# Kernel optimization log

Measured on AMD Instinct MI355X. Metric: run time of the kernel, lower is better.

The kernel has to match this reference:

```python
import jax, jax.numpy as jnp
import numpy as np

N_ITEMS = 30000
N_USERS = 20000
N_NODES = N_ITEMS + N_USERS  # 50000
N_EDGES = 512000
D0, D1, D2 = 768, 128, 64
EPS = 1e-12  # torch F.normalize eps


def _xavier(key, shape):
    fan_in, fan_out = shape
    bound = np.sqrt(6.0 / (fan_in + fan_out)).astype(np.float32)
    return jax.random.uniform(key, shape, jnp.float32, -bound, bound)


def setup_inputs() -> dict:
    key = jax.random.key(0)
    ks = jax.random.split(key, 12)
    return {
        "item_embed": jax.random.normal(ks[0], (N_ITEMS, D0), jnp.float32) * 0.05,
        "user_embed": jax.random.normal(ks[1], (N_USERS, D0), jnp.float32) * 0.05,
        "W1_0": _xavier(ks[2], (D0, D1)),
        "b1_0": jnp.zeros((D1,), jnp.float32),
        "W2_0": _xavier(ks[3], (D0, D1)),
        "b2_0": jnp.zeros((D1,), jnp.float32),
        "W1_1": _xavier(ks[4], (D1, D2)),
        "b1_1": jnp.zeros((D2,), jnp.float32),
        "W2_1": _xavier(ks[5], (D1, D2)),
        "b2_1": jnp.zeros((D2,), jnp.float32),
        # normalized-Laplacian-like positive edge weights
        "edge_vals": jax.random.uniform(ks[6], (N_EDGES,), jnp.float32) * 0.1,
        "edge_rows": jax.random.randint(ks[7], (N_EDGES,), 0, N_NODES, jnp.int32),
        "edge_cols": jax.random.randint(ks[8], (N_EDGES,), 0, N_NODES, jnp.int32),
    }


def _ngcf_layer(ego, edge_vals, edge_rows, edge_cols, W1, b1, W2, b2):
    # side = A_in @ ego : gather source features, scale, segment-sum into rows
    msg = edge_vals[:, None] * ego[edge_cols]            # (E, d) gather
    side = jax.ops.segment_sum(msg, edge_rows, num_segments=N_NODES)
    side_plus_I = side + ego                             # (A + I) @ ego
    simple = side_plus_I @ W1 + b1                       # linear1
    interaction = (side * ego) @ W2 + b2                 # linear2 on Hadamard
    return jax.nn.leaky_relu(simple + interaction)       # dropout = eval/no-op


def reference(item_embed, user_embed, W1_0, b1_0, W2_0, b2_0,
              W1_1, b1_1, W2_1, b2_1, edge_vals, edge_rows, edge_cols):
    ego = jnp.concatenate([item_embed, user_embed], axis=0)  # (N, 768)
    all_embed = [ego]
    for (W1, b1, W2, b2) in ((W1_0, b1_0, W2_0, b2_0), (W1_1, b1_1, W2_1, b2_1)):
        ego = _ngcf_layer(ego, edge_vals, edge_rows, edge_cols, W1, b1, W2, b2)
        norm = jnp.maximum(jnp.linalg.norm(ego, axis=1, keepdims=True), EPS)
        all_embed.append(ego / norm)
    return jnp.concatenate(all_embed, axis=1)  # (N, 768+128+64)
```

## Files before the change

kernel.cpp:

```cpp
#include <hip/hip_runtime.h>
#include <stdint.h>

#define N_ITEMS 30000
#define N_USERS 20000
#define N_NODES 50000
#define N_EDGES 512000
#define D0 768
#define D1 128
#define D2 64
#define OSTRIDE 960

typedef short bf16x8 __attribute__((ext_vector_type(8)));
typedef float f32x4  __attribute__((ext_vector_type(4)));
typedef unsigned short u16x4 __attribute__((ext_vector_type(4)));
typedef unsigned short u16x2 __attribute__((ext_vector_type(2)));

__device__ __forceinline__ unsigned short f2bf(float x) {
    union { float f; uint32_t u; } v; v.f = x;
    uint32_t u = v.u;
    return (unsigned short)((u + 0x7FFF + ((u >> 16) & 1)) >> 16);
}
__device__ __forceinline__ float bf2f(unsigned short s) {
    union { uint32_t u; float f; } v; v.u = ((uint32_t)s) << 16; return v.f;
}

__global__ __launch_bounds__(256) void copy_ego0(const float* __restrict__ item,
                                                 const float* __restrict__ user,
                                                 float* __restrict__ out,
                                                 unsigned short* __restrict__ outb) {
    int idx = blockIdx.x * 256 + threadIdx.x;
    if (idx >= N_NODES * (D0 / 4)) return;
    int row = idx / (D0 / 4);
    int c4  = idx % (D0 / 4);
    const float4* src = (row < N_ITEMS)
        ? (const float4*)(item + (size_t)row * D0)
        : (const float4*)(user + (size_t)(row - N_ITEMS) * D0);
    float4 v = src[c4];
    *(float4*)(out + (size_t)row * OSTRIDE + c4 * 4) = v;
    if (outb) {
        u16x4 b;
        b[0] = f2bf(v.x); b[1] = f2bf(v.y); b[2] = f2bf(v.z); b[3] = f2bf(v.w);
        *(u16x4*)(outb + (size_t)row * D0 + c4 * 4) = b;
    }
}

__global__ __launch_bounds__(256) void histogram_kernel(const int* __restrict__ rows,
                                                        int* __restrict__ counts) {
    int e = blockIdx.x * 256 + threadIdx.x;
    if (e < N_EDGES) atomicAdd(&counts[rows[e]], 1);
}

#define SCAN_THREADS 1024
__global__ __launch_bounds__(1024) void scan_kernel(const int* __restrict__ counts,
                                                    int* __restrict__ offsets,
                                                    int* __restrict__ cursors) {
    __shared__ int partials[SCAN_THREADS];
    const int CH = (N_NODES + SCAN_THREADS - 1) / SCAN_THREADS;
    int t = threadIdx.x;
    int base = t * CH;
    int sum = 0;
    for (int i = 0; i < CH; i++) {
        int idx = base + i;
        if (idx < N_NODES) sum += counts[idx];
    }
    partials[t] = sum;
    __syncthreads();
    for (int off = 1; off < SCAN_THREADS; off <<= 1) {
        int add = (t >= off) ? partials[t - off] : 0;
        __syncthreads();
        partials[t] += add;
        __syncthreads();
    }
    int run = (t == 0) ? 0 : partials[t - 1];
    for (int i = 0; i < CH; i++) {
        int idx = base + i;
        if (idx < N_NODES) {
            offsets[idx] = run;
            cursors[idx] = run;
            run += counts[idx];
        }
    }
    if (t == SCAN_THREADS - 1) offsets[N_NODES] = N_EDGES;
}

__global__ __launch_bounds__(256) void fill_kernel(const float* __restrict__ vals,
                                                   const int* __restrict__ rows,
                                                   const int* __restrict__ cols,
                                                   int* __restrict__ cursors,
                                                   float* __restrict__ svals,
                                                   int* __restrict__ scols) {
    int e = blockIdx.x * 256 + threadIdx.x;
    if (e >= N_EDGES) return;
    int pos = atomicAdd(&cursors[rows[e]], 1);
    svals[pos] = vals[e];
    scols[pos] = cols[e];
}

template <int K, int N>
__global__ __launch_bounds__(256) void prep_wb(const float* __restrict__ W,
                                               unsigned short* __restrict__ Wb) {
    constexpr int FR = (K / 32) * (N / 16);
    int tid = blockIdx.x * 256 + threadIdx.x;
    if (tid >= FR * 64) return;
    int frag = tid >> 6, lane = tid & 63;
    int kk = frag / (N / 16), nt = frag % (N / 16);
    int quad = lane >> 4, n = lane & 15;
    unsigned short tmp[8];
#pragma unroll
    for (int jj = 0; jj < 8; jj++) {
        int k = kk * 32 + quad * 8 + jj;
        tmp[jj] = f2bf(W[(size_t)k * N + nt * 16 + n]);
    }
#pragma unroll
    for (int jj = 0; jj < 8; jj++) Wb[(size_t)tid * 8 + jj] = tmp[jj];
}

template <int DIN, int DOUT, int THREADS, bool BSRC>
__global__ __launch_bounds__(THREADS) void fused_layer_mfma(
    const int*   __restrict__ offsets,
    const float* __restrict__ svals,
    const int*   __restrict__ scols,
    const float* __restrict__ ego, int ego_stride,
    const unsigned short* __restrict__ egob,
    const unsigned short* __restrict__ Wb1,
    const unsigned short* __restrict__ Wb2,
    const float* __restrict__ b1, const float* __restrict__ b2,
    float* __restrict__ out, int out_stride,
    unsigned short* __restrict__ outb)
{
    constexpr int NPB   = 16;
    constexpr int WAVES = THREADS / 64;
    constexpr int NPW   = NPB / WAVES;
    constexpr int KK    = DIN / 32;
    constexpr int NT    = DOUT / 16;
    constexpr int NTW   = NT / WAVES;
    constexpr int PAD   = 8;
    constexpr int CW    = (DIN >= 256) ? 4 : 2;
    constexpr int NC    = DIN / (64 * CW);

    __shared__ unsigned short s_sum [NPB][DIN + PAD];
    __shared__ unsigned short s_prod[NPB][DIN + PAD];

    const int t = threadIdx.x;
    const int w = t >> 6, l = t & 63;
    const int node_base = blockIdx.x * NPB;

    for (int nn = 0; nn < NPW; nn++) {
        int n   = w * NPW + nn;
        int row = node_base + n;
        int beg = offsets[row], end = offsets[row + 1];
        float acc[NC * CW];
#pragma unroll
        for (int c = 0; c < NC * CW; c++) acc[c] = 0.f;

        auto gather_one = [&](int gc, float v) {
            if constexpr (BSRC) {
                const unsigned short* sp = egob + (size_t)gc * DIN;
#pragma unroll
                for (int c = 0; c < NC; c++) {
                    if constexpr (CW == 4) {
                        u16x4 q = *(const u16x4*)(sp + c * 256 + l * 4);
#pragma unroll
                        for (int j = 0; j < 4; j++)
                            acc[c * 4 + j] = fmaf(v, bf2f(q[j]), acc[c * 4 + j]);
                    } else {
                        u16x2 q = *(const u16x2*)(sp + l * 2);
                        acc[0] = fmaf(v, bf2f(q[0]), acc[0]);
                        acc[1] = fmaf(v, bf2f(q[1]), acc[1]);
                    }
                }
            } else {
                const float* sp = ego + (size_t)gc * ego_stride;
#pragma unroll
                for (int c = 0; c < NC; c++) {
                    if constexpr (CW == 4) {
                        float4 q = *(const float4*)(sp + c * 256 + l * 4);
                        acc[c * 4 + 0] = fmaf(v, q.x, acc[c * 4 + 0]);
                        acc[c * 4 + 1] = fmaf(v, q.y, acc[c * 4 + 1]);
                        acc[c * 4 + 2] = fmaf(v, q.z, acc[c * 4 + 2]);
                        acc[c * 4 + 3] = fmaf(v, q.w, acc[c * 4 + 3]);
                    } else {
                        float2 q = *(const float2*)(sp + l * 2);
                        acc[0] = fmaf(v, q.x, acc[0]);
                        acc[1] = fmaf(v, q.y, acc[1]);
                    }
                }
            }
        };

        for (int base = beg; base < end; base += 64) {
            int cnt = min(64, end - base);
            int   cl = 0;
            float vl = 0.f;
            if (l < cnt) { cl = scols[base + l]; vl = svals[base + l]; }
            int u = 0;
            for (; u + 1 < cnt; u += 2) {
                int   g0 = __shfl(cl, u),     g1 = __shfl(cl, u + 1);
                float v0 = __shfl(vl, u),     v1 = __shfl(vl, u + 1);
                gather_one(g0, v0);
                gather_one(g1, v1);
            }
            if (u < cnt) gather_one(__shfl(cl, u), __shfl(vl, u));
        }

#pragma unroll
        for (int c = 0; c < NC; c++) {
            if constexpr (CW == 4) {
                float4 e4 = *(const float4*)(ego + (size_t)row * ego_stride + c * 256 + l * 4);
                float eg[4] = {e4.x, e4.y, e4.z, e4.w};
                u16x4 s, p;
#pragma unroll
                for (int j = 0; j < 4; j++) {
                    float a = acc[c * 4 + j];
                    s[j] = f2bf(a + eg[j]);
                    p[j] = f2bf(a * eg[j]);
                }
                *(u16x4*)&s_sum [n][c * 256 + l * 4] = s;
                *(u16x4*)&s_prod[n][c * 256 + l * 4] = p;
            } else {
                float2 e2 = *(const float2*)(ego + (size_t)row * ego_stride + l * 2);
                u16x2 s, p;
                s[0] = f2bf(acc[0] + e2.x); p[0] = f2bf(acc[0] * e2.x);
                s[1] = f2bf(acc[1] + e2.y); p[1] = f2bf(acc[1] * e2.y);
                *(u16x2*)&s_sum [n][l * 2] = s;
                *(u16x2*)&s_prod[n][l * 2] = p;
            }
        }
    }
    __syncthreads();

    const int m = l & 15, quad = l >> 4;
    f32x4 accc[NTW] = {};
    for (int kk = 0; kk < KK; kk++) {
        bf16x8 a_s = *(const bf16x8*)&s_sum [m][kk * 32 + quad * 8];
        bf16x8 a_p = *(const bf16x8*)&s_prod[m][kk * 32 + quad * 8];
#pragma unroll
        for (int i = 0; i < NTW; i++) {
            int nt = w * NTW + i;
            bf16x8 bf1 = *(const bf16x8*)(Wb1 + ((size_t)(kk * NT + nt) * 64 + l) * 8);
            bf16x8 bf2 = *(const bf16x8*)(Wb2 + ((size_t)(kk * NT + nt) * 64 + l) * 8);
            accc[i] = __builtin_amdgcn_mfma_f32_16x16x32_bf16(a_s, bf1, accc[i], 0, 0, 0);
            accc[i] = __builtin_amdgcn_mfma_f32_16x16x32_bf16(a_p, bf2, accc[i], 0, 0, 0);
        }
    }

#pragma unroll
    for (int i = 0; i < NTW; i++) {
        int nt = w * NTW + i;
        int j  = nt * 16 + m;
        float bb = b1[j] + b2[j];
#pragma unroll
        for (int r = 0; r < 4; r++) {
            int node  = node_base + quad * 4 + r;
            float val = accc[i][r] + bb;
            val = val > 0.f ? val : 0.01f * val;
            out[(size_t)node * out_stride + j] = val;
            if (outb) outb[(size_t)node * DOUT + j] = f2bf(val);
        }
    }
}

__global__ __launch_bounds__(64) void normalize_kernel(float* __restrict__ out) {
    int row  = blockIdx.x;
    int lane = threadIdx.x;
    float* p1 = out + (size_t)row * OSTRIDE + D0;
    float* p2 = p1 + D1;

    float2 v = *(float2*)(p1 + lane * 2);
    float ss = v.x * v.x + v.y * v.y;
#pragma unroll
    for (int off = 32; off > 0; off >>= 1) ss += __shfl_xor(ss, off, 64);
    float inv1 = 1.0f / fmaxf(sqrtf(ss), 1e-12f);
    v.x *= inv1; v.y *= inv1;
    *(float2*)(p1 + lane * 2) = v;

    float wv = p2[lane];
    float ss2 = wv * wv;
#pragma unroll
    for (int off = 32; off > 0; off >>= 1) ss2 += __shfl_xor(ss2, off, 64);
    p2[lane] = wv / fmaxf(sqrtf(ss2), 1e-12f);
}

extern "C" void kernel_launch(void* const* d_in, const int* in_sizes, int n_in,
                              void* d_out, int out_size, void* d_ws, size_t ws_size,
                              hipStream_t stream) {
    const float* item  = (const float*)d_in[0];
    const float* user  = (const float*)d_in[1];
    const float* W1_0  = (const float*)d_in[2];
    const float* b1_0  = (const float*)d_in[3];
    const float* W2_0  = (const float*)d_in[4];
    const float* b2_0  = (const float*)d_in[5];
    const float* W1_1  = (const float*)d_in[6];
    const float* b1_1  = (const float*)d_in[7];
    const float* W2_1  = (const float*)d_in[8];
    const float* b2_1  = (const float*)d_in[9];
    const float* evals = (const float*)d_in[10];
    const int*   erows = (const int*)d_in[11];
    const int*   ecols = (const int*)d_in[12];
    float* out = (float*)d_out;

    int*   counts  = (int*)d_ws;
    int*   offsets = counts + N_NODES;
    int*   cursors = offsets + (N_NODES + 1);
    float* svals   = (float*)((int*)d_ws + 150004);
    int*   scols   = (int*)(svals + N_EDGES);
    unsigned short* wb1_0 = (unsigned short*)(scols + N_EDGES);
    unsigned short* wb2_0 = wb1_0 + (size_t)D0 * D1;
    unsigned short* wb1_1 = wb2_0 + (size_t)D0 * D1;
    unsigned short* wb2_1 = wb1_1 + (size_t)D1 * D2;
    unsigned short* ego0b = wb2_1 + (size_t)D1 * D2;
    unsigned short* ego1b = ego0b + (size_t)N_NODES * D0;

    const size_t need = 5122000 + (size_t)N_NODES * D0 * 2 + (size_t)N_NODES * D1 * 2;
    const bool big = ws_size >= need;

    copy_ego0<<<(N_NODES * (D0 / 4) + 255) / 256, 256, 0, stream>>>(
        item, user, out, big ? ego0b : nullptr);

    hipMemsetAsync(counts, 0, (size_t)N_NODES * sizeof(int), stream);
    histogram_kernel<<<(N_EDGES + 255) / 256, 256, 0, stream>>>(erows, counts);
    scan_kernel<<<1, SCAN_THREADS, 0, stream>>>(counts, offsets, cursors);
    fill_kernel<<<(N_EDGES + 255) / 256, 256, 0, stream>>>(evals, erows, ecols,
                                                           cursors, svals, scols);

    {
        constexpr int FR0 = (D0 / 32) * (D1 / 16);
        constexpr int FR1 = (D1 / 32) * (D2 / 16);
        prep_wb<D0, D1><<<(FR0 * 64 + 255) / 256, 256, 0, stream>>>(W1_0, wb1_0);
        prep_wb<D0, D1><<<(FR0 * 64 + 255) / 256, 256, 0, stream>>>(W2_0, wb2_0);
        prep_wb<D1, D2><<<(FR1 * 64 + 255) / 256, 256, 0, stream>>>(W1_1, wb1_1);
        prep_wb<D1, D2><<<(FR1 * 64 + 255) / 256, 256, 0, stream>>>(W2_1, wb2_1);
    }

    if (big) {
        fused_layer_mfma<D0, D1, 512, true><<<N_NODES / 16, 512, 0, stream>>>(
            offsets, svals, scols, out, OSTRIDE, ego0b,
            wb1_0, wb2_0, b1_0, b2_0, out + D0, OSTRIDE, ego1b);
        fused_layer_mfma<D1, D2, 256, true><<<N_NODES / 16, 256, 0, stream>>>(
            offsets, svals, scols, out + D0, OSTRIDE, ego1b,
            wb1_1, wb2_1, b1_1, b2_1, out + D0 + D1, OSTRIDE, nullptr);
    } else {
        fused_layer_mfma<D0, D1, 512, false><<<N_NODES / 16, 512, 0, stream>>>(
            offsets, svals, scols, out, OSTRIDE, nullptr,
            wb1_0, wb2_0, b1_0, b2_0, out + D0, OSTRIDE, nullptr);
        fused_layer_mfma<D1, D2, 256, false><<<N_NODES / 16, 256, 0, stream>>>(
            offsets, svals, scols, out + D0, OSTRIDE, nullptr,
            wb1_1, wb2_1, b1_1, b2_1, out + D0 + D1, OSTRIDE, nullptr);
    }

    normalize_kernel<<<N_NODES, 64, 0, stream>>>(out);
}
```

Baseline: 718.2 us.

## Unroll bf16 gather by four edges with wider loads and pack normalize blocks

Specializes the bf16 gather paths for DIN=768 and DIN=128. Each iteration now handles four edges, issuing all loads before the FMAs, and the 768-wide path uses 16-byte plus 8-byte vector loads per lane. The self-term now comes from the bf16 copy instead of the fp32 output. The change also adds an occupancy hint to launch_bounds and packs four rows per 256-thread block in the normalize kernel to cut block count. The aim is more memory-level parallelism in the latency-bound gather, at the cost of more registers per lane and a slight precision change in the self-term.

```diff
diff --git a/kernel.cpp b/kernel.cpp
--- a/kernel.cpp
+++ b/kernel.cpp
@@ -12,6 +12,7 @@
 
 typedef short bf16x8 __attribute__((ext_vector_type(8)));
 typedef float f32x4  __attribute__((ext_vector_type(4)));
+typedef unsigned short u16x8 __attribute__((ext_vector_type(8)));
 typedef unsigned short u16x4 __attribute__((ext_vector_type(4)));
 typedef unsigned short u16x2 __attribute__((ext_vector_type(2)));
 
@@ -116,7 +117,7 @@
 }
 
 template <int DIN, int DOUT, int THREADS, bool BSRC>
-__global__ __launch_bounds__(THREADS) void fused_layer_mfma(
+__global__ __launch_bounds__(THREADS, (THREADS == 512 ? 6 : 4)) void fused_layer_mfma(
     const int*   __restrict__ offsets,
     const float* __restrict__ svals,
     const int*   __restrict__ scols,
@@ -135,8 +136,6 @@
     constexpr int NT    = DOUT / 16;
     constexpr int NTW   = NT / WAVES;
     constexpr int PAD   = 8;
-    constexpr int CW    = (DIN >= 256) ? 4 : 2;
-    constexpr int NC    = DIN / (64 * CW);
 
     __shared__ unsigned short s_sum [NPB][DIN + PAD];
     __shared__ unsigned short s_prod[NPB][DIN + PAD];
@@ -149,81 +148,152 @@
         int n   = w * NPW + nn;
         int row = node_base + n;
         int beg = offsets[row], end = offsets[row + 1];
-        float acc[NC * CW];
-#pragma unroll
-        for (int c = 0; c < NC * CW; c++) acc[c] = 0.f;
-
-        auto gather_one = [&](int gc, float v) {
-            if constexpr (BSRC) {
-                const unsigned short* sp = egob + (size_t)gc * DIN;
-#pragma unroll
-                for (int c = 0; c < NC; c++) {
-                    if constexpr (CW == 4) {
-                        u16x4 q = *(const u16x4*)(sp + c * 256 + l * 4);
-#pragma unroll
-                        for (int j = 0; j < 4; j++)
-                            acc[c * 4 + j] = fmaf(v, bf2f(q[j]), acc[c * 4 + j]);
-                    } else {
-                        u16x2 q = *(const u16x2*)(sp + l * 2);
-                        acc[0] = fmaf(v, bf2f(q[0]), acc[0]);
-                        acc[1] = fmaf(v, bf2f(q[1]), acc[1]);
+
+        if constexpr (BSRC && DIN == 768) {
+            u16x8 eg0 = *(const u16x8*)(egob + (size_t)row * 768 + l * 8);
+            u16x4 eg1 = *(const u16x4*)(egob + (size_t)row * 768 + 512 + l * 4);
+            float acc0[8] = {0.f, 0.f, 0.f, 0.f, 0.f, 0.f, 0.f, 0.f};
+            float acc1[4] = {0.f, 0.f, 0.f, 0.f};
+
+            for (int base = beg; base < end; base += 64) {
+                int cnt = min(64, end - base);
+                int   cl = 0;
+                float vl = 0.f;
+                if (l < cnt) { cl = scols[base + l]; vl = svals[base + l]; }
+                int u = 0;
+                for (; u + 4 <= cnt; u += 4) {
+                    const unsigned short* sp0 = egob + (size_t)__shfl(cl, u + 0) * 768;
+                    const unsigned short* sp1 = egob + (size_t)__shfl(cl, u + 1) * 768;
+                    const unsigned short* sp2 = egob + (size_t)__shfl(cl, u + 2) * 768;
+                    const unsigned short* sp3 = egob + (size_t)__shfl(cl, u + 3) * 768;
+                    float v0 = __shfl(vl, u + 0), v1 = __shfl(vl, u + 1);
+                    float v2 = __shfl(vl, u + 2), v3 = __shfl(vl, u + 3);
+                    u16x8 a0 = *(const u16x8*)(sp0 + l * 8);
+                    u16x8 a1 = *(const u16x8*)(sp1 + l * 8);
+                    u16x8 a2 = *(const u16x8*)(sp2 + l * 8);
+                    u16x8 a3 = *(const u16x8*)(sp3 + l * 8);
+                    u16x4 c0 = *(const u16x4*)(sp0 + 512 + l * 4);
+                    u16x4 c1 = *(const u16x4*)(sp1 + 512 + l * 4);
+                    u16x4 c2 = *(const u16x4*)(sp2 + 512 + l * 4);
+                    u16x4 c3 = *(const u16x4*)(sp3 + 512 + l * 4);
+#pragma unroll
+                    for (int j = 0; j < 8; j++) {
+                        acc0[j] = fmaf(v0, bf2f(a0[j]), acc0[j]);
+                        acc0[j] = fmaf(v1, bf2f(a1[j]), acc0[j]);
+                        acc0[j] = fmaf(v2, bf2f(a2[j]), acc0[j]);
+                        acc0[j] = fmaf(v3, bf2f(a3[j]), acc0[j]);
+                    }
+#pragma unroll
+                    for (int j = 0; j < 4; j++) {
+                        acc1[j] = fmaf(v0, bf2f(c0[j]), acc1[j]);
+                        acc1[j] = fmaf(v1, bf2f(c1[j]), acc1[j]);
+                        acc1[j] = fmaf(v2, bf2f(c2[j]), acc1[j]);
+                        acc1[j] = fmaf(v3, bf2f(c3[j]), acc1[j]);
                     }
                 }
-            } else {
-                const float* sp = ego + (size_t)gc * ego_stride;
-#pragma unroll
-                for (int c = 0; c < NC; c++) {
-                    if constexpr (CW == 4) {
-                        float4 q = *(const float4*)(sp + c * 256 + l * 4);
-                        acc[c * 4 + 0] = fmaf(v, q.x, acc[c * 4 + 0]);
-                        acc[c * 4 + 1] = fmaf(v, q.y, acc[c * 4 + 1]);
-                        acc[c * 4 + 2] = fmaf(v, q.z, acc[c * 4 + 2]);
-                        acc[c * 4 + 3] = fmaf(v, q.w, acc[c * 4 + 3]);
-                    } else {
-                        float2 q = *(const float2*)(sp + l * 2);
-                        acc[0] = fmaf(v, q.x, acc[0]);
-                        acc[1] = fmaf(v, q.y, acc[1]);
+                for (; u < cnt; u++) {
+                    const unsigned short* sp = egob + (size_t)__shfl(cl, u) * 768;
+                    float v0 = __shfl(vl, u);
+                    u16x8 a0 = *(const u16x8*)(sp + l * 8);
+                    u16x4 c0 = *(const u16x4*)(sp + 512 + l * 4);
+#pragma unroll
+                    for (int j = 0; j < 8; j++) acc0[j] = fmaf(v0, bf2f(a0[j]), acc0[j]);
+#pragma unroll
+                    for (int j = 0; j < 4; j++) acc1[j] = fmaf(v0, bf2f(c0[j]), acc1[j]);
+                }
+            }
+            u16x8 s0, p0; u16x4 s1, p1;
+#pragma unroll
+            for (int j = 0; j < 8; j++) {
+                float e = bf2f(eg0[j]);
+                s0[j] = f2bf(acc0[j] + e);
+                p0[j] = f2bf(acc0[j] * e);
+            }
+#pragma unroll
+            for (int j = 0; j < 4; j++) {
+                float e = bf2f(eg1[j]);
+                s1[j] = f2bf(acc1[j] + e);
+                p1[j] = f2bf(acc1[j] * e);
+            }
+            *(u16x8*)&s_sum [n][l * 8] = s0;
+            *(u16x8*)&s_prod[n][l * 8] = p0;
+            *(u16x4*)&s_sum [n][512 + l * 4] = s1;
+            *(u16x4*)&s_prod[n][512 + l * 4] = p1;
+        } else if constexpr (BSRC && DIN == 128) {
+            u16x2 eg = *(const u16x2*)(egob + (size_t)row * 128 + l * 2);
+            float acc[2] = {0.f, 0.f};
+            for (int base = beg; base < end; base += 64) {
+                int cnt = min(64, end - base);
+                int   cl = 0;
+                float vl = 0.f;
+                if (l < cnt) { cl = scols[base + l]; vl = svals[base + l]; }
+                int u = 0;
+                for (; u + 4 <= cnt; u += 4) {
+                    const unsigned short* sp0 = egob + (size_t)__shfl(cl, u + 0) * 128;
+                    const unsigned short* sp1 = egob + (size_t)__shfl(cl, u + 1) * 128;
+                    const unsigned short* sp2 = egob + (size_t)__shfl(cl, u + 2) * 128;
+                    const unsigned short* sp3 = egob + (size_t)__shfl(cl, u + 3) * 128;
+                    float v0 = __shfl(vl, u + 0), v1 = __shfl(vl, u + 1);
+                    float v2 = __shfl(vl, u + 2), v3 = __shfl(vl, u + 3);
+                    u16x2 a0 = *(const u16x2*)(sp0 + l * 2);
+                    u16x2 a1 = *(const u16x2*)(sp1 + l * 2);
+                    u16x2 a2 = *(const u16x2*)(sp2 + l * 2);
+                    u16x2 a3 = *(const u16x2*)(sp3 + l * 2);
+#pragma unroll
+                    for (int j = 0; j < 2; j++) {
+                        acc[j] = fmaf(v0, bf2f(a0[j]), acc[j]);
+                        acc[j] = fmaf(v1, bf2f(a1[j]), acc[j]);
+                        acc[j] = fmaf(v2, bf2f(a2[j]), acc[j]);
+                        acc[j] = fmaf(v3, bf2f(a3[j]), acc[j]);
                     }
                 }
-            }
-        };
-
-        for (int base = beg; base < end; base += 64) {
-            int cnt = min(64, end - base);
-            int   cl = 0;
-            float vl = 0.f;
-            if (l < cnt) { cl = scols[base + l]; vl = svals[base + l]; }
-            int u = 0;
-            for (; u + 1 < cnt; u += 2) {
-                int   g0 = __shfl(cl, u),     g1 = __shfl(cl, u + 1);
-                float v0 = __shfl(vl, u),     v1 = __shfl(vl, u + 1);
-                gather_one(g0, v0);
-                gather_one(g1, v1);
-            }
-            if (u < cnt) gather_one(__shfl(cl, u), __shfl(vl, u));
-        }
-
-#pragma unroll
-        for (int c = 0; c < NC; c++) {
-            if constexpr (CW == 4) {
-                float4 e4 = *(const float4*)(ego + (size_t)row * ego_stride + c * 256 + l * 4);
-                float eg[4] = {e4.x, e4.y, e4.z, e4.w};
-                u16x4 s, p;
-#pragma unroll
-                for (int j = 0; j < 4; j++) {
-                    float a = acc[c * 4 + j];
-                    s[j] = f2bf(a + eg[j]);
-                    p[j] = f2bf(a * eg[j]);
+                for (; u < cnt; u++) {
+                    const unsigned short* sp = egob + (size_t)__shfl(cl, u) * 128;
+                    float v0 = __shfl(vl, u);
+                    u16x2 a0 = *(const u16x2*)(sp + l * 2);
+                    acc[0] = fmaf(v0, bf2f(a0[0]), acc[0]);
+                    acc[1] = fmaf(v0, bf2f(a0[1]), acc[1]);
                 }
-                *(u16x4*)&s_sum [n][c * 256 + l * 4] = s;
-                *(u16x4*)&s_prod[n][c * 256 + l * 4] = p;
-            } else {
-                float2 e2 = *(const float2*)(ego + (size_t)row * ego_stride + l * 2);
-                u16x2 s, p;
-                s[0] = f2bf(acc[0] + e2.x); p[0] = f2bf(acc[0] * e2.x);
-                s[1] = f2bf(acc[1] + e2.y); p[1] = f2bf(acc[1] * e2.y);
-                *(u16x2*)&s_sum [n][l * 2] = s;
-                *(u16x2*)&s_prod[n][l * 2] = p;
+            }
+            u16x2 s, p;
+            float e0 = bf2f(eg[0]), e1 = bf2f(eg[1]);
+            s[0] = f2bf(acc[0] + e0); p[0] = f2bf(acc[0] * e0);
+            s[1] = f2bf(acc[1] + e1); p[1] = f2bf(acc[1] * e1);
+            *(u16x2*)&s_sum [n][l * 2] = s;
+            *(u16x2*)&s_prod[n][l * 2] = p;
+        } else {
+            constexpr int CW = (DIN >= 256) ? 4 : 2;
+            constexpr int NC = DIN / (64 * CW);
+            float acc[NC * CW], eg[NC * CW];
+#pragma unroll
+            for (int c = 0; c < NC * CW; c++) acc[c] = 0.f;
+#pragma unroll
+            for (int c = 0; c < NC; c++) {
+#pragma unroll
+                for (int j = 0; j < CW; j++)
+                    eg[c * CW + j] = ego[(size_t)row * ego_stride + c * 64 * CW + l * CW + j];
+            }
+            for (int base = beg; base < end; base += 64) {
+                int cnt = min(64, end - base);
+                int   cl = 0;
+                float vl = 0.f;
+                if (l < cnt) { cl = scols[base + l]; vl = svals[base + l]; }
+                for (int u = 0; u < cnt; u++) {
+                    const float* sp = ego + (size_t)__shfl(cl, u) * ego_stride;
+                    float v0 = __shfl(vl, u);
+#pragma unroll
+                    for (int c = 0; c < NC; c++) {
+#pragma unroll
+                        for (int j = 0; j < CW; j++)
+                            acc[c * CW + j] = fmaf(v0, sp[c * 64 * CW + l * CW + j], acc[c * CW + j]);
+                    }
+                }
+            }
+#pragma unroll
+            for (int c = 0; c < NC * CW; c++) {
+                int col = (c / CW) * 64 * CW + l * CW + (c % CW);
+                s_sum [n][col] = f2bf(acc[c] + eg[c]);
+                s_prod[n][col] = f2bf(acc[c] * eg[c]);
             }
         }
     }
@@ -260,9 +330,9 @@
     }
 }
 
-__global__ __launch_bounds__(64) void normalize_kernel(float* __restrict__ out) {
-    int row  = blockIdx.x;
-    int lane = threadIdx.x;
+__global__ __launch_bounds__(256) void normalize_kernel(float* __restrict__ out) {
+    int row  = blockIdx.x * 4 + (threadIdx.x >> 6);
+    int lane = threadIdx.x & 63;
     float* p1 = out + (size_t)row * OSTRIDE + D0;
     float* p2 = p1 + D1;
 
@@ -348,5 +418,5 @@
             wb1_1, wb2_1, b1_1, b2_1, out + D0 + D1, OSTRIDE, nullptr);
     }
 
-    normalize_kernel<<<N_NODES, 64, 0, stream>>>(out);
-}
+    normalize_kernel<<<N_NODES / 4, 256, 0, stream>>>(out);
+}
```

Measured after the change: 705.4 us. About the same (-1.8%).
